# Performance work log

Hardware: AMD Instinct MI355X
Metric: run time of the kernel (lower is better)

## Reference

```python
import jax, jax.numpy as jnp
import numpy as np

EPS = 1e-8  # torch.nn.CosineSimilarity default eps


def setup_inputs() -> dict:
    key = jax.random.key(0)
    mapping = jax.random.normal(key, (8192, 512), dtype=jnp.float32)
    return {"mapping": mapping}


def reference(mapping) -> jnp.ndarray:
    # Pairwise cosine distance: 1 - (x_i . x_j) / max(||x_i||*||x_j||, eps)
    # Efficient form: single N x D GEMM + outer product of norms
    dots = mapping @ mapping.T                      # [N, N]
    norms = jnp.linalg.norm(mapping, axis=-1)       # [N]
    denom = jnp.maximum(norms[:, None] * norms[None, :], EPS)
    return 1.0 - dots / denom
```

## Files before the change

### kernel.cpp

```cpp
#include <hip/hip_runtime.h>

typedef __attribute__((ext_vector_type(8))) short bf16x8;
typedef __attribute__((ext_vector_type(8))) unsigned short u16x8;
typedef __attribute__((ext_vector_type(4))) float f32x4;

__device__ __forceinline__ unsigned short f2bf(float f) {
    unsigned int u = __float_as_uint(f);
    u += 0x7fffu + ((u >> 16) & 1u);
    return (unsigned short)(u >> 16);
}

__global__ __launch_bounds__(256) void normalize_rows(
    const float* __restrict__ X, unsigned short* __restrict__ Y) {
    const int wave = threadIdx.x >> 6;
    const int lane = threadIdx.x & 63;
    const long row = (long)blockIdx.x * 4 + wave;

    const float4* xr = (const float4*)(X + row * 512);
    float4 a = xr[lane * 2];
    float4 b = xr[lane * 2 + 1];

    float s = a.x * a.x + a.y * a.y + a.z * a.z + a.w * a.w
            + b.x * b.x + b.y * b.y + b.z * b.z + b.w * b.w;
#pragma unroll
    for (int off = 32; off; off >>= 1) s += __shfl_xor(s, off, 64);

    const float inv = rsqrtf(s);

    u16x8 o;
    o[0] = f2bf(a.x * inv); o[1] = f2bf(a.y * inv);
    o[2] = f2bf(a.z * inv); o[3] = f2bf(a.w * inv);
    o[4] = f2bf(b.x * inv); o[5] = f2bf(b.y * inv);
    o[6] = f2bf(b.z * inv); o[7] = f2bf(b.w * inv);
    ((u16x8*)(Y + row * 512))[lane] = o;
}

#define GLDS16(g, l)                                                         \
    __builtin_amdgcn_global_load_lds(                                        \
        (const __attribute__((address_space(1))) void*)(g),                  \
        (__attribute__((address_space(3))) void*)(l), 16, 0, 0)

__global__ __launch_bounds__(256) void cosdist_gemm_sym(
    const unsigned short* __restrict__ Y, float* __restrict__ out) {
    constexpr int N = 8192, K = 512, BM = 128, BK = 32;
    constexpr int NTI = N / BM;
    constexpr int A2 = 2 * NTI + 1;

    __shared__ __align__(16) short As[BM * BK];
    __shared__ __align__(16) short Bs[BM * BK];

    const int p = blockIdx.x;
    int bi = (int)floorf((A2 - sqrtf((float)(A2 * A2) - 8.0f * (float)p)) * 0.5f);
    while ((bi + 1) * (A2 - (bi + 1)) / 2 <= p) ++bi;
    while (bi * (A2 - bi) / 2 > p) --bi;
    const int bj = bi + (p - bi * (A2 - bi) / 2);
    const int bm = bi * BM;
    const int bn = bj * BM;

    const int tid  = threadIdx.x;
    const int lane = tid & 63;
    const int wave = tid >> 6;
    const int wr = wave >> 1, wc = wave & 1;

    f32x4 acc[4][4] = {};

    const int c0 = tid, c1 = tid + 256;
    const unsigned short* Ag0 = Y + (size_t)(bm + (c0 >> 2)) * K + ((c0 & 3) << 3);
    const unsigned short* Ag1 = Y + (size_t)(bm + (c1 >> 2)) * K + ((c1 & 3) << 3);
    const unsigned short* Bg0 = Y + (size_t)(bn + (c0 >> 2)) * K + ((c0 & 3) << 3);
    const unsigned short* Bg1 = Y + (size_t)(bn + (c1 >> 2)) * K + ((c1 & 3) << 3);
    short* Al0 = As + c0 * 8;
    short* Al1 = As + c1 * 8;
    short* Bl0 = Bs + c0 * 8;
    short* Bl1 = Bs + c1 * 8;

    const int frow = lane & 15;
    const int fk   = (lane >> 4) << 3;

    for (int k0 = 0; k0 < K; k0 += BK) {
        GLDS16(Ag0 + k0, Al0);
        GLDS16(Ag1 + k0, Al1);
        GLDS16(Bg0 + k0, Bl0);
        GLDS16(Bg1 + k0, Bl1);
        __syncthreads();

        bf16x8 af[4], bfr[4];
#pragma unroll
        for (int t = 0; t < 4; ++t) {
            af[t]  = *(const bf16x8*)&As[(wr * 64 + t * 16 + frow) * BK + fk];
            bfr[t] = *(const bf16x8*)&Bs[(wc * 64 + t * 16 + frow) * BK + fk];
        }
#pragma unroll
        for (int mt = 0; mt < 4; ++mt)
#pragma unroll
            for (int nt = 0; nt < 4; ++nt)
                acc[mt][nt] = __builtin_amdgcn_mfma_f32_16x16x32_bf16(
                    af[mt], bfr[nt], acc[mt][nt], 0, 0, 0);
        __syncthreads();
    }

    const int crow0 = wr * 64 + ((lane >> 4) << 2);
    const int ccol0 = wc * 64 + (lane & 15);
    const bool offdiag = (bm != bn);

#pragma unroll
    for (int mt = 0; mt < 4; ++mt)
#pragma unroll
        for (int nt = 0; nt < 4; ++nt) {
            f32x4 v;
#pragma unroll
            for (int r = 0; r < 4; ++r) v[r] = 1.0f - acc[mt][nt][r];
            const int row = bm + crow0 + mt * 16;
            const int col = bn + ccol0 + nt * 16;

            *(f32x4*)&out[(size_t)col * N + row] = v;

            if (offdiag) {
#pragma unroll
                for (int r = 0; r < 4; ++r)
                    out[(size_t)(row + r) * N + col] = v[r];
            }
        }
}

extern "C" void kernel_launch(void* const* d_in, const int* in_sizes, int n_in,
                              void* d_out, int out_size, void* d_ws, size_t ws_size,
                              hipStream_t stream) {
    const float* X = (const float*)d_in[0];
    float* out = (float*)d_out;
    unsigned short* Y = (unsigned short*)d_ws;

    const int D = 512;
    const int N = in_sizes[0] / D;

    normalize_rows<<<N / 4, 256, 0, stream>>>(X, Y);

    const int nt = N / 128;
    const int ntiles = nt * (nt + 1) / 2;
    cosdist_gemm_sym<<<ntiles, 256, 0, stream>>>(Y, out);
}
```

Measured before the change: 348.1 us.

## Use 256x256 tiles with double-buffered swizzled LDS and XCD-aware tile mapping

Rewrites the symmetric GEMM to use 256x256 output tiles with 512 threads, K-steps of 64, and double-buffered LDS. Prefetch of the next K slice is split into quarters interleaved with MFMA phases, using s_setprio and barriers. LDS columns are XOR-swizzled to avoid bank conflicts, and block IDs are remapped across the 8 XCDs. The larger tiles halve the number of global loads per output element. In exchange the kernel uses more registers and LDS, and there are far fewer workgroups (528) to spread over the CUs.

Measured after the change: 372.4 us. 1.07x slower.

```diff
diff --git a/kernel.cpp b/kernel.cpp
--- a/kernel.cpp
+++ b/kernel.cpp
@@ -40,78 +40,171 @@
         (const __attribute__((address_space(1))) void*)(g),                  \
         (__attribute__((address_space(3))) void*)(l), 16, 0, 0)
 
-__global__ __launch_bounds__(256) void cosdist_gemm_sym(
+#define RD(base, r, c) \
+    (*(const bf16x8*)((base) + (r) * 64 + ((((c) ^ ((r) & 7))) << 3)))
+
+__global__ __launch_bounds__(512, 2) void cosdist_gemm_sym(
     const unsigned short* __restrict__ Y, float* __restrict__ out) {
-    constexpr int N = 8192, K = 512, BM = 128, BK = 32;
-    constexpr int NTI = N / BM;
-    constexpr int A2 = 2 * NTI + 1;
-
-    __shared__ __align__(16) short As[BM * BK];
-    __shared__ __align__(16) short Bs[BM * BK];
-
-    const int p = blockIdx.x;
-    int bi = (int)floorf((A2 - sqrtf((float)(A2 * A2) - 8.0f * (float)p)) * 0.5f);
+    constexpr int N = 8192, K = 512, BM = 256;
+    constexpr int NT = N / BM;
+    constexpr int A2 = 2 * NT + 1;
+    constexpr int TILE = BM * 64;
+
+    __shared__ __align__(16) short As[2 * TILE];
+    __shared__ __align__(16) short Bs[2 * TILE];
+
+    constexpr int NWG = NT * (NT + 1) / 2;
+    constexpr int CPX = NWG / 8;
+    const int hw = blockIdx.x;
+    const int p = (hw & 7) * CPX + (hw >> 3);
+
+    int bi = (int)floorf(((float)A2 - sqrtf((float)(A2 * A2) - 8.0f * (float)p)) * 0.5f);
     while ((bi + 1) * (A2 - (bi + 1)) / 2 <= p) ++bi;
     while (bi * (A2 - bi) / 2 > p) --bi;
     const int bj = bi + (p - bi * (A2 - bi) / 2);
-    const int bm = bi * BM;
-    const int bn = bj * BM;
+    const int bm = bi * BM, bn = bj * BM;
 
     const int tid  = threadIdx.x;
     const int lane = tid & 63;
     const int wave = tid >> 6;
-    const int wr = wave >> 1, wc = wave & 1;
-
-    f32x4 acc[4][4] = {};
-
-    const int c0 = tid, c1 = tid + 256;
-    const unsigned short* Ag0 = Y + (size_t)(bm + (c0 >> 2)) * K + ((c0 & 3) << 3);
-    const unsigned short* Ag1 = Y + (size_t)(bm + (c1 >> 2)) * K + ((c1 & 3) << 3);
-    const unsigned short* Bg0 = Y + (size_t)(bn + (c0 >> 2)) * K + ((c0 & 3) << 3);
-    const unsigned short* Bg1 = Y + (size_t)(bn + (c1 >> 2)) * K + ((c1 & 3) << 3);
-    short* Al0 = As + c0 * 8;
-    short* Al1 = As + c1 * 8;
-    short* Bl0 = Bs + c0 * 8;
-    short* Bl1 = Bs + c1 * 8;
-
+    const int wr = wave >> 2;
+    const int wc = wave & 3;
     const int frow = lane & 15;
-    const int fk   = (lane >> 4) << 3;
-
-    for (int k0 = 0; k0 < K; k0 += BK) {
-        GLDS16(Ag0 + k0, Al0);
-        GLDS16(Ag1 + k0, Al1);
-        GLDS16(Bg0 + k0, Bl0);
-        GLDS16(Bg1 + k0, Bl1);
-        __syncthreads();
-
-        bf16x8 af[4], bfr[4];
-#pragma unroll
-        for (int t = 0; t < 4; ++t) {
-            af[t]  = *(const bf16x8*)&As[(wr * 64 + t * 16 + frow) * BK + fk];
-            bfr[t] = *(const bf16x8*)&Bs[(wc * 64 + t * 16 + frow) * BK + fk];
-        }
-#pragma unroll
-        for (int mt = 0; mt < 4; ++mt)
-#pragma unroll
-            for (int nt = 0; nt < 4; ++nt)
-                acc[mt][nt] = __builtin_amdgcn_mfma_f32_16x16x32_bf16(
-                    af[mt], bfr[nt], acc[mt][nt], 0, 0, 0);
+    const int fch  = lane >> 4;
+
+    const int srow = tid >> 3;
+    const int sgc  = (tid & 7) ^ (srow & 7);
+    const unsigned short* Abase = Y + (size_t)(bm + srow) * K + (sgc << 3);
+    const unsigned short* Bbase = Y + (size_t)(bn + srow) * K + (sgc << 3);
+    const size_t QSTEP = (size_t)64 * K;
+
+    f32x4 acc[8][4] = {};
+
+#pragma unroll
+    for (int j = 0; j < 4; ++j) {
+        GLDS16(Abase + (size_t)j * QSTEP, As + j * 4096 + tid * 8);
+        GLDS16(Bbase + (size_t)j * QSTEP, Bs + j * 4096 + tid * 8);
+    }
+    __syncthreads();
+
+    for (int kt = 0; kt < 8; ++kt) {
+        const short* Ac = As + (kt & 1) * TILE;
+        const short* Bc = Bs + (kt & 1) * TILE;
+        short* An = As + ((kt + 1) & 1) * TILE;
+        short* Bn = Bs + ((kt + 1) & 1) * TILE;
+        const int kn = (kt + 1) << 6;
+        const bool pf = (kt < 7);
+
+        bf16x8 af[4][2], bfv[2][2];
+
+        if (pf) {
+            GLDS16(Abase + kn, An + tid * 8);
+            GLDS16(Bbase + kn, Bn + tid * 8);
+        }
+#pragma unroll
+        for (int m = 0; m < 4; ++m) {
+            const int r = wr * 128 + m * 16 + frow;
+            af[m][0] = RD(Ac, r, fch);
+            af[m][1] = RD(Ac, r, 4 + fch);
+        }
+#pragma unroll
+        for (int n = 0; n < 2; ++n) {
+            const int r = wc * 64 + n * 16 + frow;
+            bfv[n][0] = RD(Bc, r, fch);
+            bfv[n][1] = RD(Bc, r, 4 + fch);
+        }
+        __builtin_amdgcn_s_setprio(1);
+#pragma unroll
+        for (int m = 0; m < 4; ++m)
+#pragma unroll
+            for (int n = 0; n < 2; ++n)
+#pragma unroll
+                for (int kk = 0; kk < 2; ++kk)
+                    acc[m][n] = __builtin_amdgcn_mfma_f32_16x16x32_bf16(
+                        af[m][kk], bfv[n][kk], acc[m][n], 0, 0, 0);
+        __builtin_amdgcn_s_setprio(0);
+        __builtin_amdgcn_s_barrier();
+
+        if (pf) {
+            GLDS16(Abase + kn + QSTEP, An + 4096 + tid * 8);
+            GLDS16(Bbase + kn + QSTEP, Bn + 4096 + tid * 8);
+        }
+#pragma unroll
+        for (int n = 0; n < 2; ++n) {
+            const int r = wc * 64 + (n + 2) * 16 + frow;
+            bfv[n][0] = RD(Bc, r, fch);
+            bfv[n][1] = RD(Bc, r, 4 + fch);
+        }
+        __builtin_amdgcn_s_setprio(1);
+#pragma unroll
+        for (int m = 0; m < 4; ++m)
+#pragma unroll
+            for (int n = 0; n < 2; ++n)
+#pragma unroll
+                for (int kk = 0; kk < 2; ++kk)
+                    acc[m][n + 2] = __builtin_amdgcn_mfma_f32_16x16x32_bf16(
+                        af[m][kk], bfv[n][kk], acc[m][n + 2], 0, 0, 0);
+        __builtin_amdgcn_s_setprio(0);
+        __builtin_amdgcn_s_barrier();
+
+        if (pf) {
+            GLDS16(Abase + kn + 2 * QSTEP, An + 2 * 4096 + tid * 8);
+            GLDS16(Bbase + kn + 2 * QSTEP, Bn + 2 * 4096 + tid * 8);
+        }
+#pragma unroll
+        for (int m = 0; m < 4; ++m) {
+            const int r = wr * 128 + (m + 4) * 16 + frow;
+            af[m][0] = RD(Ac, r, fch);
+            af[m][1] = RD(Ac, r, 4 + fch);
+        }
+        __builtin_amdgcn_s_setprio(1);
+#pragma unroll
+        for (int m = 0; m < 4; ++m)
+#pragma unroll
+            for (int n = 0; n < 2; ++n)
+#pragma unroll
+                for (int kk = 0; kk < 2; ++kk)
+                    acc[m + 4][n + 2] = __builtin_amdgcn_mfma_f32_16x16x32_bf16(
+                        af[m][kk], bfv[n][kk], acc[m + 4][n + 2], 0, 0, 0);
+        __builtin_amdgcn_s_setprio(0);
+        __builtin_amdgcn_s_barrier();
+
+        if (pf) {
+            GLDS16(Abase + kn + 3 * QSTEP, An + 3 * 4096 + tid * 8);
+            GLDS16(Bbase + kn + 3 * QSTEP, Bn + 3 * 4096 + tid * 8);
+        }
+#pragma unroll
+        for (int n = 0; n < 2; ++n) {
+            const int r = wc * 64 + n * 16 + frow;
+            bfv[n][0] = RD(Bc, r, fch);
+            bfv[n][1] = RD(Bc, r, 4 + fch);
+        }
+        __builtin_amdgcn_s_setprio(1);
+#pragma unroll
+        for (int m = 0; m < 4; ++m)
+#pragma unroll
+            for (int n = 0; n < 2; ++n)
+#pragma unroll
+                for (int kk = 0; kk < 2; ++kk)
+                    acc[m + 4][n] = __builtin_amdgcn_mfma_f32_16x16x32_bf16(
+                        af[m][kk], bfv[n][kk], acc[m + 4][n], 0, 0, 0);
+        __builtin_amdgcn_s_setprio(0);
         __syncthreads();
     }
 
-    const int crow0 = wr * 64 + ((lane >> 4) << 2);
-    const int ccol0 = wc * 64 + (lane & 15);
+    const int rbase = bm + wr * 128 + (fch << 2);
+    const int cbase = bn + wc * 64 + frow;
     const bool offdiag = (bm != bn);
 
 #pragma unroll
-    for (int mt = 0; mt < 4; ++mt)
-#pragma unroll
-        for (int nt = 0; nt < 4; ++nt) {
+    for (int m = 0; m < 8; ++m)
+#pragma unroll
+        for (int n = 0; n < 4; ++n) {
             f32x4 v;
 #pragma unroll
-            for (int r = 0; r < 4; ++r) v[r] = 1.0f - acc[mt][nt][r];
-            const int row = bm + crow0 + mt * 16;
-            const int col = bn + ccol0 + nt * 16;
+            for (int r = 0; r < 4; ++r) v[r] = 1.0f - acc[m][n][r];
+            const int row = rbase + m * 16;
+            const int col = cbase + n * 16;
 
             *(f32x4*)&out[(size_t)col * N + row] = v;
 
@@ -135,7 +228,7 @@
 
     normalize_rows<<<N / 4, 256, 0, stream>>>(X, Y);
 
-    const int nt = N / 128;
+    const int nt = N / 256;
     const int ntiles = nt * (nt + 1) / 2;
-    cosdist_gemm_sym<<<ntiles, 256, 0, stream>>>(Y, out);
-}
+    cosdist_gemm_sym<<<ntiles, 512, 0, stream>>>(Y, out);
+}
```

## Load MFMA fragments directly from global memory, removing LDS staging and barriers

Applied to the files above, without the earlier changes.

The GEMM main loop no longer stages A and B tiles through shared memory with global_load_lds and two __syncthreads per K step. Each wave now reads its bf16x8 fragments straight from global memory (L2/L1), and the K loop is fully unrolled. This removes LDS traffic and barrier stalls and lets the compiler schedule loads early. In exchange, each tile is reloaded by both waves that share it rather than being shared through LDS, which raises cache and global load pressure and register use.

Result: slower. 416.0 us (+19.5%).

```diff
diff --git a/kernel.cpp b/kernel.cpp
--- a/kernel.cpp
+++ b/kernel.cpp
@@ -35,22 +35,14 @@
     ((u16x8*)(Y + row * 512))[lane] = o;
 }
 
-#define GLDS16(g, l)                                                         \
-    __builtin_amdgcn_global_load_lds(                                        \
-        (const __attribute__((address_space(1))) void*)(g),                  \
-        (__attribute__((address_space(3))) void*)(l), 16, 0, 0)
-
 __global__ __launch_bounds__(256) void cosdist_gemm_sym(
     const unsigned short* __restrict__ Y, float* __restrict__ out) {
-    constexpr int N = 8192, K = 512, BM = 128, BK = 32;
+    constexpr int N = 8192, K = 512, BM = 128;
     constexpr int NTI = N / BM;
     constexpr int A2 = 2 * NTI + 1;
 
-    __shared__ __align__(16) short As[BM * BK];
-    __shared__ __align__(16) short Bs[BM * BK];
-
     const int p = blockIdx.x;
-    int bi = (int)floorf((A2 - sqrtf((float)(A2 * A2) - 8.0f * (float)p)) * 0.5f);
+    int bi = (int)floorf(((float)A2 - sqrtf((float)(A2 * A2) - 8.0f * (float)p)) * 0.5f);
     while ((bi + 1) * (A2 - (bi + 1)) / 2 <= p) ++bi;
     while (bi * (A2 - bi) / 2 > p) --bi;
     const int bj = bi + (p - bi * (A2 - bi) / 2);
@@ -61,46 +53,32 @@
     const int lane = tid & 63;
     const int wave = tid >> 6;
     const int wr = wave >> 1, wc = wave & 1;
+    const int frow = lane & 15;
+    const int fk   = (lane >> 4) << 3;
+
+    const unsigned short* Ab0 = Y + (size_t)(bm + wr * 64 + frow) * K + fk;
+    const unsigned short* Bb0 = Y + (size_t)(bn + wc * 64 + frow) * K + fk;
 
     f32x4 acc[4][4] = {};
 
-    const int c0 = tid, c1 = tid + 256;
-    const unsigned short* Ag0 = Y + (size_t)(bm + (c0 >> 2)) * K + ((c0 & 3) << 3);
-    const unsigned short* Ag1 = Y + (size_t)(bm + (c1 >> 2)) * K + ((c1 & 3) << 3);
-    const unsigned short* Bg0 = Y + (size_t)(bn + (c0 >> 2)) * K + ((c0 & 3) << 3);
-    const unsigned short* Bg1 = Y + (size_t)(bn + (c1 >> 2)) * K + ((c1 & 3) << 3);
-    short* Al0 = As + c0 * 8;
-    short* Al1 = As + c1 * 8;
-    short* Bl0 = Bs + c0 * 8;
-    short* Bl1 = Bs + c1 * 8;
-
-    const int frow = lane & 15;
-    const int fk   = (lane >> 4) << 3;
-
-    for (int k0 = 0; k0 < K; k0 += BK) {
-        GLDS16(Ag0 + k0, Al0);
-        GLDS16(Ag1 + k0, Al1);
-        GLDS16(Bg0 + k0, Bl0);
-        GLDS16(Bg1 + k0, Bl1);
-        __syncthreads();
-
-        bf16x8 af[4], bfr[4];
+#pragma unroll
+    for (int k0 = 0; k0 < K; k0 += 32) {
+        bf16x8 af[4], bfv[4];
 #pragma unroll
         for (int t = 0; t < 4; ++t) {
-            af[t]  = *(const bf16x8*)&As[(wr * 64 + t * 16 + frow) * BK + fk];
-            bfr[t] = *(const bf16x8*)&Bs[(wc * 64 + t * 16 + frow) * BK + fk];
+            af[t]  = *(const bf16x8*)(Ab0 + (size_t)t * 16 * K + k0);
+            bfv[t] = *(const bf16x8*)(Bb0 + (size_t)t * 16 * K + k0);
         }
 #pragma unroll
         for (int mt = 0; mt < 4; ++mt)
 #pragma unroll
             for (int nt = 0; nt < 4; ++nt)
                 acc[mt][nt] = __builtin_amdgcn_mfma_f32_16x16x32_bf16(
-                    af[mt], bfr[nt], acc[mt][nt], 0, 0, 0);
-        __syncthreads();
+                    af[mt], bfv[nt], acc[mt][nt], 0, 0, 0);
     }
 
     const int crow0 = wr * 64 + ((lane >> 4) << 2);
-    const int ccol0 = wc * 64 + (lane & 15);
+    const int ccol0 = wc * 64 + frow;
     const bool offdiag = (bm != bn);
 
 #pragma unroll
```
